# Kernel optimization log

Hardware: AMD Instinct MI355X
Metric: run time of the kernel (lower is better)

Reference implementation:

```python
import jax, jax.numpy as jnp
import numpy as np

NUM_JOINT_LIST = [8, 10, 12, 14, 16, 18, 20, 22, 24, 9, 13, 17]
NUM_GLOBAL_LIST = [1, 0, 1, 1, 0, 1, 1, 1, 0, 1, 1, 1]
M = len(NUM_JOINT_LIST)
B, T, JMAX = 16, 128, 24
H, HEADS, L, RANK = 256, 8, 4, 8
DH = H // HEADS
LAYERSCALE = 1e-4


def setup_inputs():
    key = jax.random.key(0)
    ks = jax.random.split(key, 40)
    m_idx = jax.random.randint(ks[0], (B,), 0, M)
    nj = jnp.array(NUM_JOINT_LIST)[m_idx]
    valid = jnp.arange(JMAX)[None, :] < nj[:, None]  # (B, J) real joints of each morphology
    jtype = jax.random.randint(ks[1], (B, JMAX), 0, 3)  # 0 slide, 1 hinge, 2 global
    has_g = (jnp.array(NUM_GLOBAL_LIST) > 0)[m_idx][:, None]
    jtype = jnp.where((jtype == 2) & ~has_g, 0, jtype)
    tile = lambda m: jnp.broadcast_to(m[:, None, :], (B, T, JMAX))
    slide_mask = tile((jtype == 0) & valid)
    hinge_mask = tile((jtype == 1) & valid)
    global_mask = tile((jtype == 2) & valid)
    act_mask = tile(valid)
    morph_mask = (valid[:, :, None] & valid[:, None, :]) | jnp.eye(JMAX, dtype=bool)[None]
    act = jax.random.normal(ks[2], (B, T, JMAX, 1), dtype=jnp.float32)
    s = 0.02
    inp = dict(act=act, slide_mask=slide_mask, hinge_mask=hinge_mask,
               global_mask=global_mask, act_mask=act_mask, morph_mask=morph_mask,
               m_idx=m_idx)
    inp['Ws'] = s * jax.random.normal(ks[3], (1, H)); inp['bs'] = jnp.zeros((H,))
    inp['Wh'] = s * jax.random.normal(ks[4], (1, H)); inp['bh'] = jnp.zeros((H,))
    inp['Wg'] = s * jax.random.normal(ks[5], (M, H))
    inp['Wact'] = s * jax.random.normal(ks[6], (1, H))
    pos = jax.random.normal(ks[7], (M, JMAX, H))
    pos_valid = jnp.arange(JMAX)[None, :, None] < jnp.array(NUM_JOINT_LIST)[:, None, None]
    inp['pos'] = pos * pos_valid  # rows beyond num_joint stay zero, as in the torch loop
    inp['ln1_s'] = jnp.ones((L, H)); inp['ln1_b'] = jnp.zeros((L, H))
    inp['Wqkv'] = s * jax.random.normal(ks[8], (L, H, 3 * H)); inp['bqkv'] = jnp.zeros((L, 3 * H))
    inp['loraA'] = s * jax.random.normal(ks[9], (L, M, H, RANK))
    inp['loraB'] = s * jax.random.normal(ks[10], (L, M, RANK, 3 * H))
    inp['Wo'] = s * jax.random.normal(ks[11], (L, H, H)); inp['bo'] = jnp.zeros((L, H))
    inp['ln2_s'] = jnp.ones((L, H)); inp['ln2_b'] = jnp.zeros((L, H))
    inp['W1'] = s * jax.random.normal(ks[12], (L, H, 4 * H)); inp['b1'] = jnp.zeros((L, 4 * H))
    inp['W2'] = s * jax.random.normal(ks[13], (L, 4 * H, H)); inp['b2'] = jnp.zeros((L, H))
    inp['g1'] = LAYERSCALE * jnp.ones((L, H)); inp['g2'] = LAYERSCALE * jnp.ones((L, H))
    inp['lnf_s'] = jnp.ones((H,)); inp['lnf_b'] = jnp.zeros((H,))
    return inp


def _ln(z, sc, bi):
    mu = z.mean(-1, keepdims=True)
    v = ((z - mu) ** 2).mean(-1, keepdims=True)
    return (z - mu) * jax.lax.rsqrt(v + 1e-5) * sc + bi


def reference(act, slide_mask, hinge_mask, global_mask, act_mask, morph_mask, m_idx,
              Ws, bs, Wh, bh, Wg, Wact, pos,
              ln1_s, ln1_b, Wqkv, bqkv, loraA, loraB, Wo, bo,
              ln2_s, ln2_b, W1, b1, W2, b2, g1, g2, lnf_s, lnf_b):
    has_g = (jnp.array(NUM_GLOBAL_LIST) > 0)[m_idx]  # (B,)
    a1 = act[..., :1]  # slide_dim = hinge_dim = num_global = 1
    emb = jnp.where(slide_mask[..., None], a1 @ Ws + bs, jnp.zeros((), act.dtype))
    emb = jnp.where(hinge_mask[..., None], a1 @ Wh + bh, emb)
    emb_g = a1 * Wg[m_idx][:, None, None, :]  # per-sample morphology-routed projection
    emb = jnp.where((global_mask & has_g[:, None, None])[..., None], emb_g, emb)
    y = emb + act_mask[..., None].astype(emb.dtype) * Wact[0]
    y = y + pos[m_idx][:, None]  # (B, T, J, H)
    Bv, Tv, J, _ = y.shape
    N = Bv * Tv
    x = y.reshape(N, J, H)
    amask = jnp.broadcast_to(morph_mask[:, None], (Bv, Tv, J, J)).reshape(N, J, J)
    t_idx = jnp.repeat(m_idx, Tv)  # (N,)
    neg = jnp.finfo(x.dtype).min
    scale = 1.0 / np.sqrt(DH)

    def block(x, lp):
        l1s, l1b, wqkv, bq, lA, lB, wo, bo_, l2s, l2b, w1, b1_, w2, b2_, gg1, gg2 = lp
        h = _ln(x, l1s, l1b)
        qkv = h @ wqkv + bq
        # per-task LoRA on qkv, gathered by morphology index
        qkv = qkv + jnp.einsum('njr,nrk->njk', jnp.einsum('njd,ndr->njr', h, lA[t_idx]), lB[t_idx])
        q, k, v = jnp.split(qkv, 3, axis=-1)
        q = q.reshape(N, J, HEADS, DH).transpose(0, 2, 1, 3)
        k = k.reshape(N, J, HEADS, DH).transpose(0, 2, 1, 3)
        v = v.reshape(N, J, HEADS, DH).transpose(0, 2, 1, 3)
        scores = jnp.einsum('nhid,nhjd->nhij', q, k) * scale
        scores = jnp.where(amask[:, None], scores, neg)
        attn = jax.nn.softmax(scores, axis=-1)
        o = jnp.einsum('nhij,nhjd->nhid', attn, v).transpose(0, 2, 1, 3).reshape(N, J, H)
        x = x + gg1 * (o @ wo + bo_)
        h2 = _ln(x, l2s, l2b)
        x = x + gg2 * (jax.nn.gelu(h2 @ w1 + b1_) @ w2 + b2_)
        return x, None

    x, _ = jax.lax.scan(block, x, (ln1_s, ln1_b, Wqkv, bqkv, loraA, loraB, Wo, bo,
                                   ln2_s, ln2_b, W1, b1, W2, b2, g1, g2))
    x = _ln(x, lnf_s, lnf_b)
    return x.reshape(Bv, Tv, J, H)
```

## Files before the change

### kernel.cpp

```cpp
#include <hip/hip_runtime.h>
#include <cstdint>
#include <cstddef>

#define B_     16
#define T_     128
#define J_     24
#define H_     256
#define HEADS_ 8
#define DH_    32
#define L_     4
#define RANK_  8
#define M_     12
#define NTOK   (B_*T_)
#define ROWS   (NTOK*J_)
#define KQ     320
#define HAS_G_MASK 3821

typedef __attribute__((ext_vector_type(8))) short short8;
typedef __attribute__((ext_vector_type(4))) float f32x4;

__constant__ int cNJ[M_] = {8, 10, 12, 14, 16, 18, 20, 22, 24, 9, 13, 17};

__device__ __forceinline__ float bf2f(unsigned short u) {
    union { unsigned int i; float f; } c; c.i = ((unsigned int)u) << 16; return c.f;
}
__device__ __forceinline__ unsigned short f2bf(float f) {
    union { float f; unsigned int i; } c; c.f = f;
    unsigned int x = c.i;
    return (unsigned short)((x + 0x7fffu + ((x >> 16) & 1u)) >> 16);
}
__device__ __forceinline__ float asf(unsigned int u) {
    union { unsigned int i; float f; } c; c.i = u; return c.f;
}
__device__ __forceinline__ unsigned int cvtpk(float lo, float hi) {
    unsigned int r;
    asm("v_cvt_pk_bf16_f32 %0, %1, %2" : "=v"(r) : "v"(lo), "v"(hi));
    return r;
}
__device__ __forceinline__ void gload16(const void* g, void* l) {
    __builtin_amdgcn_global_load_lds((const __attribute__((address_space(1))) void*)g,
                                     (__attribute__((address_space(3))) void*)l, 16, 0, 0);
}
#define SWZ(r) ((((r) >> 1) & 3) << 4)

__global__ void zero_flag(int* f) { *f = 0; }

__global__ __launch_bounds__(256) void detect_kernel(
    const unsigned char* __restrict__ sl, const unsigned char* __restrict__ hi,
    const unsigned char* __restrict__ gl, const int* __restrict__ m_idx,
    int* __restrict__ flag) {
    int rj = blockIdx.x * 256 + threadIdx.x;
    if (rj >= ROWS) return;
    int b = rj / (T_ * J_);
    int j = rj % J_;
    int valid = (j < cNJ[m_idx[b]]) ? 1 : 0;
    int cnt = (sl[rj] != 0) + (hi[rj] != 0) + (gl[rj] != 0);
    if (cnt != valid) atomicOr(flag, 1);
}

__global__ void wconv_t(const float* __restrict__ W, unsigned short* __restrict__ WT,
                        int K, int Nc, int total) {
    int i = blockIdx.x * 256 + threadIdx.x;
    if (i >= total) return;
    int kn = K * Nc;
    int l = i / kn;
    int r = i - l * kn;
    int n = r / K;
    int k = r - n * K;
    WT[i] = f2bf(W[(size_t)l * kn + (size_t)k * Nc + n]);
}

__global__ void wconv_qkv(const float* __restrict__ Wqkv, const float* __restrict__ loraB,
                          unsigned short* __restrict__ OT) {
    int i = blockIdx.x * 256 + threadIdx.x;
    const int total = L_ * M_ * 768 * KQ;
    if (i >= total) return;
    int k = i % KQ;
    int n = (i / KQ) % 768;
    int m = (i / (KQ * 768)) % M_;
    int l = i / (KQ * 768 * M_);
    float v = 0.f;
    if (k < 256)      v = Wqkv[((size_t)l * 256 + k) * 768 + n];
    else if (k < 264) v = loraB[(((size_t)l * M_ + m) * RANK_ + (k - 256)) * 768 + n];
    OT[i] = f2bf(v);
}

__global__ __launch_bounds__(256) void embed_kernel(
    const float* __restrict__ act, const void* __restrict__ slide,
    const void* __restrict__ hinge, const void* __restrict__ glob,
    const int* __restrict__ m_idx, const int* __restrict__ flag,
    const float* __restrict__ Ws, const float* __restrict__ bs,
    const float* __restrict__ Wh, const float* __restrict__ bh,
    const float* __restrict__ Wg, const float* __restrict__ Wact,
    const float* __restrict__ pos, float* __restrict__ X) {
    int rj = (blockIdx.x << 2) + (threadIdx.x >> 6);
    int lane = threadIdx.x & 63;
    int b = rj / (T_ * J_);
    int j = rj % J_;
    int m = m_idx[b];
    bool valid = j < cNJ[m];
    bool s, hh, gl;
    if (*flag) {
        s  = ((const int*)slide)[rj] != 0;
        hh = ((const int*)hinge)[rj] != 0;
        gl = ((const int*)glob)[rj]  != 0;
    } else {
        s  = ((const unsigned char*)slide)[rj] != 0;
        hh = ((const unsigned char*)hinge)[rj] != 0;
        gl = ((const unsigned char*)glob)[rj]  != 0;
    }
    float a1 = act[rj];
    int h0 = lane << 2;
    float e0 = 0.f, e1 = 0.f, e2 = 0.f, e3 = 0.f;
    if (s) {
        float4 w = *(const float4*)(Ws + h0); float4 bb = *(const float4*)(bs + h0);
        e0 = a1 * w.x + bb.x; e1 = a1 * w.y + bb.y; e2 = a1 * w.z + bb.z; e3 = a1 * w.w + bb.w;
    } else if (hh) {
        float4 w = *(const float4*)(Wh + h0); float4 bb = *(const float4*)(bh + h0);
        e0 = a1 * w.x + bb.x; e1 = a1 * w.y + bb.y; e2 = a1 * w.z + bb.z; e3 = a1 * w.w + bb.w;
    } else if (gl && ((HAS_G_MASK >> m) & 1)) {
        float4 w = *(const float4*)(Wg + m * H_ + h0);
        e0 = a1 * w.x; e1 = a1 * w.y; e2 = a1 * w.z; e3 = a1 * w.w;
    }
    if (valid) {
        float4 wa = *(const float4*)(Wact + h0);
        e0 += wa.x; e1 += wa.y; e2 += wa.z; e3 += wa.w;
    }
    float4 pv = *(const float4*)(pos + (size_t)(m * J_ + j) * H_ + h0);
    float4 out; out.x = e0 + pv.x; out.y = e1 + pv.y; out.z = e2 + pv.z; out.w = e3 + pv.w;
    *(float4*)(X + ((size_t)rj << 8) + h0) = out;
}

template<bool LORA>
__global__ __launch_bounds__(256) void ln_kernel(
    const float* __restrict__ X, const float* __restrict__ sc, const float* __restrict__ bi,
    const float* __restrict__ lA, const int* __restrict__ m_idx,
    unsigned short* __restrict__ Hbf, int ldh) {
    int row = (blockIdx.x << 2) + (threadIdx.x >> 6);
    int lane = threadIdx.x & 63;
    int h0 = lane << 2;
    float4 xv = *(const float4*)(X + ((size_t)row << 8) + h0);
    float s1 = xv.x + xv.y + xv.z + xv.w;
    float s2 = xv.x * xv.x + xv.y * xv.y + xv.z * xv.z + xv.w * xv.w;
    #pragma unroll
    for (int o = 32; o; o >>= 1) { s1 += __shfl_xor(s1, o); s2 += __shfl_xor(s2, o); }
    float mu = s1 * (1.f / H_);
    float var = s2 * (1.f / H_) - mu * mu;
    float rs = rsqrtf(var + 1e-5f);
    float4 scv = *(const float4*)(sc + h0);
    float4 biv = *(const float4*)(bi + h0);
    float hn0 = (xv.x - mu) * rs * scv.x + biv.x;
    float hn1 = (xv.y - mu) * rs * scv.y + biv.y;
    float hn2 = (xv.z - mu) * rs * scv.z + biv.z;
    float hn3 = (xv.w - mu) * rs * scv.w + biv.w;
    ushort4 o4; o4.x = f2bf(hn0); o4.y = f2bf(hn1); o4.z = f2bf(hn2); o4.w = f2bf(hn3);
    *(ushort4*)(Hbf + (size_t)row * ldh + h0) = o4;
    if (LORA) {
        int t = m_idx[row / (J_ * T_)];
        const float* Ap = lA + (size_t)t * (H_ * RANK_) + h0 * RANK_;
        float4 av[8];
        #pragma unroll
        for (int c = 0; c < 8; ++c) av[c] = ((const float4*)Ap)[c];
        float hn[4] = {hn0, hn1, hn2, hn3};
        float p[RANK_];
        #pragma unroll
        for (int k = 0; k < RANK_; ++k) p[k] = 0.f;
        #pragma unroll
        for (int i = 0; i < 4; ++i)
            #pragma unroll
            for (int k = 0; k < RANK_; ++k) {
                int idx = i * RANK_ + k;
                float a = (idx & 3) == 0 ? av[idx >> 2].x : (idx & 3) == 1 ? av[idx >> 2].y
                        : (idx & 3) == 2 ? av[idx >> 2].z : av[idx >> 2].w;
                p[k] += hn[i] * a;
            }
        #pragma unroll
        for (int k = 0; k < RANK_; ++k)
            #pragma unroll
            for (int o = 32; o; o >>= 1) p[k] += __shfl_xor(p[k], o);
        unsigned int w0 = (unsigned int)f2bf(p[0]) | ((unsigned int)f2bf(p[1]) << 16);
        unsigned int w1 = (unsigned int)f2bf(p[2]) | ((unsigned int)f2bf(p[3]) << 16);
        unsigned int w2 = (unsigned int)f2bf(p[4]) | ((unsigned int)f2bf(p[5]) << 16);
        unsigned int w3 = (unsigned int)f2bf(p[6]) | ((unsigned int)f2bf(p[7]) << 16);
        unsigned int tv = 0;
        if (lane == 0) tv = w0; else if (lane == 1) tv = w1;
        else if (lane == 2) tv = w2; else if (lane == 3) tv = w3;
        if (lane < 32)
            *((unsigned int*)(Hbf + (size_t)row * ldh + 256) + lane) = tv;
    }
}

__global__ __launch_bounds__(256) void lnf_kernel(
    float* __restrict__ X, const float* __restrict__ sc, const float* __restrict__ bi) {
    int row = (blockIdx.x << 2) + (threadIdx.x >> 6);
    int lane = threadIdx.x & 63;
    int h0 = lane << 2;
    float4 xv = *(const float4*)(X + ((size_t)row << 8) + h0);
    float s1 = xv.x + xv.y + xv.z + xv.w;
    float s2 = xv.x * xv.x + xv.y * xv.y + xv.z * xv.z + xv.w * xv.w;
    #pragma unroll
    for (int o = 32; o; o >>= 1) { s1 += __shfl_xor(s1, o); s2 += __shfl_xor(s2, o); }
    float mu = s1 * (1.f / H_);
    float var = s2 * (1.f / H_) - mu * mu;
    float rs = rsqrtf(var + 1e-5f);
    float4 scv = *(const float4*)(sc + h0);
    float4 biv = *(const float4*)(bi + h0);
    float4 out;
    out.x = (xv.x - mu) * rs * scv.x + biv.x;
    out.y = (xv.y - mu) * rs * scv.y + biv.y;
    out.z = (xv.z - mu) * rs * scv.z + biv.z;
    out.w = (xv.w - mu) * rs * scv.w + biv.w;
    *(float4*)(X + ((size_t)row << 8) + h0) = out;
}

template<int EPI, int K, int NC>
__global__ __launch_bounds__(256) void gemm_k(
    const unsigned short* __restrict__ A, const unsigned short* __restrict__ BT,
    const float* __restrict__ bias,
    const float* __restrict__ aux1,
    const int* __restrict__ m_idx,
    unsigned short* __restrict__ outB, float* __restrict__ outF) {
    __shared__ __align__(16) char LAs[2][8192];
    __shared__ __align__(16) char LBs[2][8192];
    char* LA0 = &LAs[0][0]; char* LA1 = &LAs[1][0];
    char* LB0 = &LBs[0][0]; char* LB1 = &LBs[1][0];
    int gx = gridDim.x;
    int nwg = gx * gridDim.y;
    int id = blockIdx.y * gx + blockIdx.x;
    int bx = blockIdx.x, by = blockIdx.y;
    {
        int q8 = nwg >> 3;
        int sid = (id & 7) * q8 + (id >> 3);
        bx = sid % gx; by = sid / gx;
    }
    int col0 = bx * 128;
    int row0 = by * 128;
    int tid = threadIdx.x;
    int wv = tid >> 6, lane = tid & 63;
    int wm = wv >> 1, wn = wv & 1;

    const unsigned short* BTe = BT;
    if (EPI == 0) BTe += (size_t)m_idx[row0 / (J_ * T_)] * (768 * KQ);

    int srow  = tid >> 2;
    int sbyte = (tid & 3) << 4;
    int sce   = (sbyte ^ SWZ(srow)) >> 1;
    const unsigned short* Ab = A   + (size_t)(row0 + srow) * K + sce;
    const unsigned short* Bb = BTe + (size_t)(col0 + srow) * K + sce;
    const size_t rstep = (size_t)64 * K;

    int ko2   = (lane >> 4) << 4;
    int rdoff = ko2 ^ SWZ(lane & 15);
    int rowA0 = wm * 64 + (lane & 15);
    int rowB0 = wn * 64 + (lane & 15);

    f32x4 acc[4][4];
    const f32x4 z = {0.f, 0.f, 0.f, 0.f};
    #pragma unroll
    for (int mi = 0; mi < 4; ++mi)
        #pragma unroll
        for (int ni = 0; ni < 4; ++ni) acc[mi][ni] = z;

    constexpr int NT = K >> 5;

    auto STAGE = [&](int kt, int b) {
        const unsigned short* a = Ab + (kt << 5);
        const unsigned short* bb = Bb + (kt << 5);
        char* la = (b ? LA1 : LA0) + (tid << 4);
        char* lb = (b ? LB1 : LB0) + (tid << 4);
        gload16(a, la);          gload16(a + rstep, la + 4096);
        gload16(bb, lb);         gload16(bb + rstep, lb + 4096);
    };
    auto COMPUTE = [&](const char* pa, const char* pb) {
        short8 af[4], bfr[4];
        #pragma unroll
        for (int q = 0; q < 4; ++q) {
            af[q]  = *(const short8*)(pa + (rowA0 + q * 16) * 64 + rdoff);
            bfr[q] = *(const short8*)(pb + (rowB0 + q * 16) * 64 + rdoff);
        }
        #pragma unroll
        for (int mi = 0; mi < 4; ++mi)
            #pragma unroll
            for (int ni = 0; ni < 4; ++ni)
                acc[mi][ni] = __builtin_amdgcn_mfma_f32_16x16x32_bf16(bfr[ni], af[mi], acc[mi][ni], 0, 0, 0);
    };

    STAGE(0, 0);
    for (int t = 0; t < NT; t += 2) {
        if (t + 1 < NT) { STAGE(t + 1, 1); asm volatile("s_waitcnt vmcnt(4)" ::: "memory"); }
        else            { asm volatile("s_waitcnt vmcnt(0)" ::: "memory"); }
        __builtin_amdgcn_s_barrier();
        __builtin_amdgcn_sched_barrier(0);
        COMPUTE(LA0, LB0);
        __builtin_amdgcn_sched_barrier(0);
        __builtin_amdgcn_s_barrier();
        if (t + 2 < NT) { STAGE(t + 2, 0); asm volatile("s_waitcnt vmcnt(4)" ::: "memory"); }
        else            { asm volatile("s_waitcnt vmcnt(0)" ::: "memory"); }
        __builtin_amdgcn_s_barrier();
        __builtin_amdgcn_sched_barrier(0);
        COMPUTE(LA1, LB1);
        __builtin_amdgcn_sched_barrier(0);
        __builtin_amdgcn_s_barrier();
    }

    int rb = row0 + wm * 64 + (lane & 15);
    int cb = col0 + wn * 64 + ((lane >> 4) << 2);

    if (EPI == 0 || EPI == 1) {
        #pragma unroll
        for (int mi = 0; mi < 4; ++mi) {
            int row = rb + mi * 16;
            #pragma unroll
            for (int ni = 0; ni < 4; ++ni) {
                int col = cb + ni * 16;
                float4 bv = *(const float4*)(bias + col);
                float v[4] = {acc[mi][ni][0] + bv.x, acc[mi][ni][1] + bv.y,
                              acc[mi][ni][2] + bv.z, acc[mi][ni][3] + bv.w};
                if (EPI == 1) {
                    #pragma unroll
                    for (int r = 0; r < 4; ++r) {
                        float u = v[r];
                        float tt = u * u;
                        float pp = fmaf(tt, 0.044715f, 1.0f) * u;
                        float e = __expf(-1.5957691216057308f * pp);
                        v[r] = u / (1.f + e);
                    }
                }
                uint2 st; st.x = cvtpk(v[0], v[1]); st.y = cvtpk(v[2], v[3]);
                *(uint2*)(outB + (size_t)row * NC + col) = st;
            }
        }
    } else {
        #pragma unroll
        for (int mi = 0; mi < 4; ++mi) {
            int row = rb + mi * 16;
            #pragma unroll
            for (int ni = 0; ni < 4; ++ni) {
                int col = cb + ni * 16;
                float4 g = *(const float4*)(aux1 + col);
                float4 bv = *(const float4*)(bias + col);
                float4 x = *(float4*)(outF + (size_t)row * H_ + col);
                x.x += g.x * (acc[mi][ni][0] + bv.x);
                x.y += g.y * (acc[mi][ni][1] + bv.y);
                x.z += g.z * (acc[mi][ni][2] + bv.z);
                x.w += g.w * (acc[mi][ni][3] + bv.w);
                *(float4*)(outF + (size_t)row * H_ + col) = x;
            }
        }
    }
}

__global__ __launch_bounds__(256) void attn_kernel(
    const unsigned short* __restrict__ QKV, const int* __restrict__ m_idx,
    unsigned short* __restrict__ O) {
    __shared__ unsigned int q2s[4][24][18];
    __shared__ unsigned int k2s[4][16][26];
    __shared__ unsigned int v2s[4][24][18];
    __shared__ float       scs[4][24][27];
    int w = threadIdx.x >> 6, lane = threadIdx.x & 63;
    int n = blockIdx.x >> 1;
    int hd = ((blockIdx.x & 1) << 2) + w;
    int nj = cNJ[m_idx[n >> 7]];
    unsigned int (*q2)[18] = q2s[w];
    unsigned int (*k2)[26] = k2s[w];
    unsigned int (*v2)[18] = v2s[w];
    float (*sc)[27] = scs[w];

    const unsigned short* base = QKV + (size_t)n * (J_ * 768) + hd * DH_;

    #pragma unroll
    for (int it = 0; it < 3; ++it) {
        int r = it * 64 + lane;
        int j = r >> 3, d0 = (r & 7) << 2, d2 = d0 >> 1;
        ushort4 x = *(const ushort4*)(base + (size_t)j * 768 + d0);
        q2[j][d2]     = (unsigned int)x.x | ((unsigned int)x.y << 16);
        q2[j][d2 + 1] = (unsigned int)x.z | ((unsigned int)x.w << 16);
    }
    #pragma unroll
    for (int it = 0; it < 3; ++it) {
        int r = it * 64 + lane;
        int j = r >> 3, d0 = (r & 7) << 2, d2 = d0 >> 1;
        ushort4 x = *(const ushort4*)(base + (size_t)j * 768 + 256 + d0);
        k2[d2][j]     = (unsigned int)x.x | ((unsigned int)x.y << 16);
        k2[d2 + 1][j] = (unsigned int)x.z | ((unsigned int)x.w << 16);
    }
    #pragma unroll
    for (int it = 0; it < 3; ++it) {
        int r = it * 64 + lane;
        int j = r >> 3, d0 = (r & 7) << 2, d2 = d0 >> 1;
        ushort4 x = *(const ushort4*)(base + (size_t)j * 768 + 512 + d0);
        v2[j][d2]     = (unsigned int)x.x | ((unsigned int)x.y << 16);
        v2[j][d2 + 1] = (unsigned int)x.z | ((unsigned int)x.w << 16);
    }

    int i = lane >> 1, half = lane & 1;
    if (lane < 48) {
        float qf[32];
        #pragma unroll
        for (int d2 = 0; d2 < 16; ++d2) {
            unsigned int x = q2[i][d2];
            qf[2 * d2]     = asf(x << 16);
            qf[2 * d2 + 1] = asf(x & 0xffff0000u);
        }
        int jb = half * 12;
        float s[12];
        #pragma unroll
        for (int jj = 0; jj < 12; ++jj) {
            int j = jb + jj;
            float acc = 0.f;
            #pragma unroll
            for (int d2 = 0; d2 < 16; ++d2) {
                unsigned int x = k2[d2][j];
                acc += qf[2 * d2] * asf(x << 16);
                acc += qf[2 * d2 + 1] * asf(x & 0xffff0000u);
            }
            bool ok = (i < nj && j < nj) || (i == j);
            s[jj] = ok ? acc * 0.17677669529663687f : -1e30f;
        }
        float mx = s[0];
        #pragma unroll
        for (int jj = 1; jj < 12; ++jj) mx = fmaxf(mx, s[jj]);
        mx = fmaxf(mx, __shfl_xor(mx, 1));
        float sm = 0.f;
        #pragma unroll
        for (int jj = 0; jj < 12; ++jj) { float e = __expf(s[jj] - mx); s[jj] = e; sm += e; }
        sm += __shfl_xor(sm, 1);
        float inv = 1.f / sm;
        #pragma unroll
        for (int jj = 0; jj < 12; ++jj) sc[i][jb + jj] = s[jj] * inv;
    }

    #pragma unroll
    for (int it = 0; it < 6; ++it) {
        int i2 = it * 4 + (lane >> 4), d2 = lane & 15;
        float olo = 0.f, ohi = 0.f;
        #pragma unroll
        for (int j = 0; j < J_; ++j) {
            float p = sc[i2][j];
            unsigned int x = v2[j][d2];
            olo += p * asf(x << 16);
            ohi += p * asf(x & 0xffff0000u);
        }
        unsigned int o = (unsigned int)f2bf(olo) | ((unsigned int)f2bf(ohi) << 16);
        *(unsigned int*)(O + (size_t)(n * J_ + i2) * H_ + hd * DH_ + 2 * d2) = o;
    }
}

extern "C" void kernel_launch(void* const* d_in, const int* in_sizes, int n_in,
                              void* d_out, int out_size, void* d_ws, size_t ws_size,
                              hipStream_t stream) {
    (void)in_sizes; (void)n_in; (void)out_size; (void)ws_size;
    const float* act   = (const float*)d_in[0];
    const void*  slide = d_in[1];
    const void*  hinge = d_in[2];
    const void*  glob  = d_in[3];
    const int* m_idx  = (const int*)d_in[6];
    const float* Ws   = (const float*)d_in[7];
    const float* bs   = (const float*)d_in[8];
    const float* Wh   = (const float*)d_in[9];
    const float* bh   = (const float*)d_in[10];
    const float* Wg   = (const float*)d_in[11];
    const float* Wact = (const float*)d_in[12];
    const float* pos  = (const float*)d_in[13];
    const float* ln1s = (const float*)d_in[14];
    const float* ln1b = (const float*)d_in[15];
    const float* Wqkv = (const float*)d_in[16];
    const float* bqkv = (const float*)d_in[17];
    const float* loraA= (const float*)d_in[18];
    const float* loraB= (const float*)d_in[19];
    const float* Wo   = (const float*)d_in[20];
    const float* bo   = (const float*)d_in[21];
    const float* ln2s = (const float*)d_in[22];
    const float* ln2b = (const float*)d_in[23];
    const float* W1   = (const float*)d_in[24];
    const float* b1   = (const float*)d_in[25];
    const float* W2   = (const float*)d_in[26];
    const float* b2   = (const float*)d_in[27];
    const float* g1   = (const float*)d_in[28];
    const float* g2   = (const float*)d_in[29];
    const float* lnfs = (const float*)d_in[30];
    const float* lnfb = (const float*)d_in[31];

    float* X = (float*)d_out;

    size_t off = 0;
    char* ws = (char*)d_ws;
    auto nxt = [&](size_t bytes) -> char* {
        char* p = ws + off; off += (bytes + 255) & ~(size_t)255; return p;
    };
    int*            dflag  = (int*)nxt(256);
    unsigned short* Hbf    = (unsigned short*)nxt((size_t)ROWS * KQ * 2);
    unsigned short* QKVG   = (unsigned short*)nxt((size_t)ROWS * 1024 * 2);
    unsigned short* WqkvTp = (unsigned short*)nxt((size_t)L_ * M_ * 768 * KQ * 2);
    unsigned short* WoT    = (unsigned short*)nxt((size_t)L_ * H_ * H_ * 2);
    unsigned short* W1T    = (unsigned short*)nxt((size_t)L_ * H_ * 1024 * 2);
    unsigned short* W2T    = (unsigned short*)nxt((size_t)L_ * 1024 * H_ * 2);
    unsigned short* Obf    = Hbf;

    zero_flag<<<1, 1, 0, stream>>>(dflag);
    detect_kernel<<<(ROWS + 255) / 256, 256, 0, stream>>>(
        (const unsigned char*)slide, (const unsigned char*)hinge,
        (const unsigned char*)glob, m_idx, dflag);

    wconv_qkv<<<(L_ * M_ * 768 * KQ + 255) / 256, 256, 0, stream>>>(Wqkv, loraB, WqkvTp);
    wconv_t<<<(L_ * H_ * H_   + 255) / 256, 256, 0, stream>>>(Wo, WoT, H_, H_,   L_ * H_ * H_);
    wconv_t<<<(L_ * H_ * 1024 + 255) / 256, 256, 0, stream>>>(W1, W1T, H_, 1024, L_ * H_ * 1024);
    wconv_t<<<(L_ * 1024 * H_ + 255) / 256, 256, 0, stream>>>(W2, W2T, 1024, H_, L_ * 1024 * H_);

    embed_kernel<<<ROWS / 4, 256, 0, stream>>>(act, slide, hinge, glob, m_idx, dflag,
                                               Ws, bs, Wh, bh, Wg, Wact, pos, X);

    for (int l = 0; l < L_; ++l) {
        ln_kernel<true><<<ROWS / 4, 256, 0, stream>>>(X, ln1s + l * H_, ln1b + l * H_,
                                                      loraA + (size_t)l * M_ * H_ * RANK_, m_idx, Hbf, KQ);
        gemm_k<0, KQ, 768><<<dim3(6, 384), 256, 0, stream>>>(Hbf, WqkvTp + (size_t)l * M_ * 768 * KQ,
                                                             bqkv + l * 768, nullptr, m_idx,
                                                             QKVG, nullptr);
        attn_kernel<<<NTOK * 2, 256, 0, stream>>>(QKVG, m_idx, Obf);
        gemm_k<2, 256, 256><<<dim3(2, 384), 256, 0, stream>>>(Obf, WoT + (size_t)l * H_ * H_,
                                                              bo + l * H_, g1 + l * H_, m_idx,
                                                              nullptr, X);
        ln_kernel<false><<<ROWS / 4, 256, 0, stream>>>(X, ln2s + l * H_, ln2b + l * H_,
                                                       nullptr, nullptr, Hbf, H_);
        gemm_k<1, 256, 1024><<<dim3(8, 384), 256, 0, stream>>>(Hbf, W1T + (size_t)l * H_ * 1024,
                                                               b1 + l * 1024, nullptr, m_idx,
                                                               QKVG, nullptr);
        gemm_k<2, 1024, 256><<<dim3(2, 384), 256, 0, stream>>>(QKVG, W2T + (size_t)l * 1024 * H_,
                                                               b2 + l * H_, g2 + l * H_, m_idx,
                                                               nullptr, X);
    }

    lnf_kernel<<<ROWS / 4, 256, 0, stream>>>(X, lnfs, lnfb);
}
```

Measured before the change: 1.380 ms.

## Fuse residual GEMMs with following LayerNorm and fold first LN into embed

Adds a full-row resid_gemm kernel: each block owns 64 rows across all 256 columns, so it can apply the residual update and then the next LayerNorm (ln2, the next layer's ln1, or the final LN) in its epilogue. The first ln1 plus its LoRA projection is folded into the embedding kernel, and a light lora_tail kernel computes the LoRA-A products from the bf16 LN output. This removes the separate LN passes over the fp32 residual stream and several launches per layer. The cost is a narrower-tiled GEMM with a cross-wave shared-memory reduction, LoRA-A computed from bf16-rounded activations, and a GELU exp now written with exp2f.

New measurement: 1.374 ms. About the same (-0.4%).

```diff
diff --git a/kernel.cpp b/kernel.cpp
--- a/kernel.cpp
+++ b/kernel.cpp
@@ -85,14 +85,16 @@
     OT[i] = f2bf(v);
 }
 
-__global__ __launch_bounds__(256) void embed_kernel(
+__global__ __launch_bounds__(256) void embed_ln_kernel(
     const float* __restrict__ act, const void* __restrict__ slide,
     const void* __restrict__ hinge, const void* __restrict__ glob,
     const int* __restrict__ m_idx, const int* __restrict__ flag,
     const float* __restrict__ Ws, const float* __restrict__ bs,
     const float* __restrict__ Wh, const float* __restrict__ bh,
     const float* __restrict__ Wg, const float* __restrict__ Wact,
-    const float* __restrict__ pos, float* __restrict__ X) {
+    const float* __restrict__ pos, const float* __restrict__ lns,
+    const float* __restrict__ lnb, const float* __restrict__ lA,
+    float* __restrict__ X, unsigned short* __restrict__ Hq) {
     int rj = (blockIdx.x << 2) + (threadIdx.x >> 6);
     int lane = threadIdx.x & 63;
     int b = rj / (T_ * J_);
@@ -127,99 +129,104 @@
         e0 += wa.x; e1 += wa.y; e2 += wa.z; e3 += wa.w;
     }
     float4 pv = *(const float4*)(pos + (size_t)(m * J_ + j) * H_ + h0);
-    float4 out; out.x = e0 + pv.x; out.y = e1 + pv.y; out.z = e2 + pv.z; out.w = e3 + pv.w;
+    float y0 = e0 + pv.x, y1 = e1 + pv.y, y2 = e2 + pv.z, y3 = e3 + pv.w;
+    float4 out; out.x = y0; out.y = y1; out.z = y2; out.w = y3;
     *(float4*)(X + ((size_t)rj << 8) + h0) = out;
-}
-
-template<bool LORA>
-__global__ __launch_bounds__(256) void ln_kernel(
-    const float* __restrict__ X, const float* __restrict__ sc, const float* __restrict__ bi,
-    const float* __restrict__ lA, const int* __restrict__ m_idx,
-    unsigned short* __restrict__ Hbf, int ldh) {
-    int row = (blockIdx.x << 2) + (threadIdx.x >> 6);
-    int lane = threadIdx.x & 63;
-    int h0 = lane << 2;
-    float4 xv = *(const float4*)(X + ((size_t)row << 8) + h0);
-    float s1 = xv.x + xv.y + xv.z + xv.w;
-    float s2 = xv.x * xv.x + xv.y * xv.y + xv.z * xv.z + xv.w * xv.w;
+
+    float s1 = y0 + y1 + y2 + y3;
+    float s2 = y0 * y0 + y1 * y1 + y2 * y2 + y3 * y3;
     #pragma unroll
     for (int o = 32; o; o >>= 1) { s1 += __shfl_xor(s1, o); s2 += __shfl_xor(s2, o); }
     float mu = s1 * (1.f / H_);
     float var = s2 * (1.f / H_) - mu * mu;
     float rs = rsqrtf(var + 1e-5f);
-    float4 scv = *(const float4*)(sc + h0);
-    float4 biv = *(const float4*)(bi + h0);
-    float hn0 = (xv.x - mu) * rs * scv.x + biv.x;
-    float hn1 = (xv.y - mu) * rs * scv.y + biv.y;
-    float hn2 = (xv.z - mu) * rs * scv.z + biv.z;
-    float hn3 = (xv.w - mu) * rs * scv.w + biv.w;
+    float4 scv = *(const float4*)(lns + h0);
+    float4 biv = *(const float4*)(lnb + h0);
+    float hn0 = (y0 - mu) * rs * scv.x + biv.x;
+    float hn1 = (y1 - mu) * rs * scv.y + biv.y;
+    float hn2 = (y2 - mu) * rs * scv.z + biv.z;
+    float hn3 = (y3 - mu) * rs * scv.w + biv.w;
     ushort4 o4; o4.x = f2bf(hn0); o4.y = f2bf(hn1); o4.z = f2bf(hn2); o4.w = f2bf(hn3);
-    *(ushort4*)(Hbf + (size_t)row * ldh + h0) = o4;
-    if (LORA) {
-        int t = m_idx[row / (J_ * T_)];
-        const float* Ap = lA + (size_t)t * (H_ * RANK_) + h0 * RANK_;
-        float4 av[8];
-        #pragma unroll
-        for (int c = 0; c < 8; ++c) av[c] = ((const float4*)Ap)[c];
-        float hn[4] = {hn0, hn1, hn2, hn3};
-        float p[RANK_];
-        #pragma unroll
-        for (int k = 0; k < RANK_; ++k) p[k] = 0.f;
-        #pragma unroll
-        for (int i = 0; i < 4; ++i)
-            #pragma unroll
-            for (int k = 0; k < RANK_; ++k) {
-                int idx = i * RANK_ + k;
-                float a = (idx & 3) == 0 ? av[idx >> 2].x : (idx & 3) == 1 ? av[idx >> 2].y
-                        : (idx & 3) == 2 ? av[idx >> 2].z : av[idx >> 2].w;
-                p[k] += hn[i] * a;
-            }
-        #pragma unroll
-        for (int k = 0; k < RANK_; ++k)
-            #pragma unroll
-            for (int o = 32; o; o >>= 1) p[k] += __shfl_xor(p[k], o);
-        unsigned int w0 = (unsigned int)f2bf(p[0]) | ((unsigned int)f2bf(p[1]) << 16);
-        unsigned int w1 = (unsigned int)f2bf(p[2]) | ((unsigned int)f2bf(p[3]) << 16);
-        unsigned int w2 = (unsigned int)f2bf(p[4]) | ((unsigned int)f2bf(p[5]) << 16);
-        unsigned int w3 = (unsigned int)f2bf(p[6]) | ((unsigned int)f2bf(p[7]) << 16);
-        unsigned int tv = 0;
-        if (lane == 0) tv = w0; else if (lane == 1) tv = w1;
-        else if (lane == 2) tv = w2; else if (lane == 3) tv = w3;
-        if (lane < 32)
-            *((unsigned int*)(Hbf + (size_t)row * ldh + 256) + lane) = tv;
-    }
-}
-
-__global__ __launch_bounds__(256) void lnf_kernel(
-    float* __restrict__ X, const float* __restrict__ sc, const float* __restrict__ bi) {
+    *(ushort4*)(Hq + (size_t)rj * KQ + h0) = o4;
+
+    int t = m;
+    const float* Ap = lA + (size_t)t * (H_ * RANK_) + h0 * RANK_;
+    float4 av[8];
+    #pragma unroll
+    for (int c = 0; c < 8; ++c) av[c] = ((const float4*)Ap)[c];
+    float hn[4] = {hn0, hn1, hn2, hn3};
+    float p[RANK_];
+    #pragma unroll
+    for (int k = 0; k < RANK_; ++k) p[k] = 0.f;
+    #pragma unroll
+    for (int i = 0; i < 4; ++i)
+        #pragma unroll
+        for (int k = 0; k < RANK_; ++k) {
+            int idx = i * RANK_ + k;
+            float a = (idx & 3) == 0 ? av[idx >> 2].x : (idx & 3) == 1 ? av[idx >> 2].y
+                    : (idx & 3) == 2 ? av[idx >> 2].z : av[idx >> 2].w;
+            p[k] += hn[i] * a;
+        }
+    #pragma unroll
+    for (int k = 0; k < RANK_; ++k)
+        #pragma unroll
+        for (int o = 32; o; o >>= 1) p[k] += __shfl_xor(p[k], o);
+    unsigned int w0 = (unsigned int)f2bf(p[0]) | ((unsigned int)f2bf(p[1]) << 16);
+    unsigned int w1 = (unsigned int)f2bf(p[2]) | ((unsigned int)f2bf(p[3]) << 16);
+    unsigned int w2 = (unsigned int)f2bf(p[4]) | ((unsigned int)f2bf(p[5]) << 16);
+    unsigned int w3 = (unsigned int)f2bf(p[6]) | ((unsigned int)f2bf(p[7]) << 16);
+    unsigned int tv = 0;
+    if (lane == 0) tv = w0; else if (lane == 1) tv = w1;
+    else if (lane == 2) tv = w2; else if (lane == 3) tv = w3;
+    if (lane < 32)
+        *((unsigned int*)(Hq + (size_t)rj * KQ + 256) + lane) = tv;
+}
+
+__global__ __launch_bounds__(256) void lora_tail_kernel(
+    unsigned short* __restrict__ Hq, const float* __restrict__ lA,
+    const int* __restrict__ m_idx) {
     int row = (blockIdx.x << 2) + (threadIdx.x >> 6);
     int lane = threadIdx.x & 63;
+    int t = m_idx[row / (J_ * T_)];
     int h0 = lane << 2;
-    float4 xv = *(const float4*)(X + ((size_t)row << 8) + h0);
-    float s1 = xv.x + xv.y + xv.z + xv.w;
-    float s2 = xv.x * xv.x + xv.y * xv.y + xv.z * xv.z + xv.w * xv.w;
-    #pragma unroll
-    for (int o = 32; o; o >>= 1) { s1 += __shfl_xor(s1, o); s2 += __shfl_xor(s2, o); }
-    float mu = s1 * (1.f / H_);
-    float var = s2 * (1.f / H_) - mu * mu;
-    float rs = rsqrtf(var + 1e-5f);
-    float4 scv = *(const float4*)(sc + h0);
-    float4 biv = *(const float4*)(bi + h0);
-    float4 out;
-    out.x = (xv.x - mu) * rs * scv.x + biv.x;
-    out.y = (xv.y - mu) * rs * scv.y + biv.y;
-    out.z = (xv.z - mu) * rs * scv.z + biv.z;
-    out.w = (xv.w - mu) * rs * scv.w + biv.w;
-    *(float4*)(X + ((size_t)row << 8) + h0) = out;
+    ushort4 hv = *(const ushort4*)(Hq + (size_t)row * KQ + h0);
+    float hn[4] = {bf2f(hv.x), bf2f(hv.y), bf2f(hv.z), bf2f(hv.w)};
+    const float* Ap = lA + (size_t)t * (H_ * RANK_) + h0 * RANK_;
+    float4 av[8];
+    #pragma unroll
+    for (int c = 0; c < 8; ++c) av[c] = ((const float4*)Ap)[c];
+    float p[RANK_];
+    #pragma unroll
+    for (int k = 0; k < RANK_; ++k) p[k] = 0.f;
+    #pragma unroll
+    for (int i = 0; i < 4; ++i)
+        #pragma unroll
+        for (int k = 0; k < RANK_; ++k) {
+            int idx = i * RANK_ + k;
+            float a = (idx & 3) == 0 ? av[idx >> 2].x : (idx & 3) == 1 ? av[idx >> 2].y
+                    : (idx & 3) == 2 ? av[idx >> 2].z : av[idx >> 2].w;
+            p[k] += hn[i] * a;
+        }
+    #pragma unroll
+    for (int k = 0; k < RANK_; ++k)
+        #pragma unroll
+        for (int o = 32; o; o >>= 1) p[k] += __shfl_xor(p[k], o);
+    unsigned int w0 = (unsigned int)f2bf(p[0]) | ((unsigned int)f2bf(p[1]) << 16);
+    unsigned int w1 = (unsigned int)f2bf(p[2]) | ((unsigned int)f2bf(p[3]) << 16);
+    unsigned int w2 = (unsigned int)f2bf(p[4]) | ((unsigned int)f2bf(p[5]) << 16);
+    unsigned int w3 = (unsigned int)f2bf(p[6]) | ((unsigned int)f2bf(p[7]) << 16);
+    unsigned int tv = 0;
+    if (lane == 0) tv = w0; else if (lane == 1) tv = w1;
+    else if (lane == 2) tv = w2; else if (lane == 3) tv = w3;
+    if (lane < 32)
+        *((unsigned int*)(Hq + (size_t)row * KQ + 256) + lane) = tv;
 }
 
 template<int EPI, int K, int NC>
 __global__ __launch_bounds__(256) void gemm_k(
     const unsigned short* __restrict__ A, const unsigned short* __restrict__ BT,
-    const float* __restrict__ bias,
-    const float* __restrict__ aux1,
-    const int* __restrict__ m_idx,
-    unsigned short* __restrict__ outB, float* __restrict__ outF) {
+    const float* __restrict__ bias, const int* __restrict__ m_idx,
+    unsigned short* __restrict__ outB) {
     __shared__ __align__(16) char LAs[2][8192];
     __shared__ __align__(16) char LBs[2][8192];
     char* LA0 = &LAs[0][0]; char* LA1 = &LAs[1][0];
@@ -227,12 +234,9 @@
     int gx = gridDim.x;
     int nwg = gx * gridDim.y;
     int id = blockIdx.y * gx + blockIdx.x;
-    int bx = blockIdx.x, by = blockIdx.y;
-    {
-        int q8 = nwg >> 3;
-        int sid = (id & 7) * q8 + (id >> 3);
-        bx = sid % gx; by = sid / gx;
-    }
+    int q8 = nwg >> 3;
+    int sid = (id & 7) * q8 + (id >> 3);
+    int bx = sid % gx, by = sid / gx;
     int col0 = bx * 128;
     int row0 = by * 128;
     int tid = threadIdx.x;
@@ -249,8 +253,7 @@
     const unsigned short* Bb = BTe + (size_t)(col0 + srow) * K + sce;
     const size_t rstep = (size_t)64 * K;
 
-    int ko2   = (lane >> 4) << 4;
-    int rdoff = ko2 ^ SWZ(lane & 15);
+    int rdoff = ((lane >> 4) << 4) ^ SWZ(lane & 15);
     int rowA0 = wm * 64 + (lane & 15);
     int rowB0 = wn * 64 + (lane & 15);
 
@@ -306,45 +309,185 @@
     int rb = row0 + wm * 64 + (lane & 15);
     int cb = col0 + wn * 64 + ((lane >> 4) << 2);
 
-    if (EPI == 0 || EPI == 1) {
-        #pragma unroll
-        for (int mi = 0; mi < 4; ++mi) {
-            int row = rb + mi * 16;
+    #pragma unroll
+    for (int mi = 0; mi < 4; ++mi) {
+        int row = rb + mi * 16;
+        #pragma unroll
+        for (int ni = 0; ni < 4; ++ni) {
+            int col = cb + ni * 16;
+            float4 bv = *(const float4*)(bias + col);
+            float v[4] = {acc[mi][ni][0] + bv.x, acc[mi][ni][1] + bv.y,
+                          acc[mi][ni][2] + bv.z, acc[mi][ni][3] + bv.w};
+            if (EPI == 1) {
+                #pragma unroll
+                for (int r = 0; r < 4; ++r) {
+                    float u = v[r];
+                    float tt = u * u;
+                    float pp = fmaf(tt, 0.044715f, 1.0f) * u;
+                    float e = exp2f(-2.3025850929940457f * pp);
+                    v[r] = u / (1.f + e);
+                }
+            }
+            uint2 st; st.x = cvtpk(v[0], v[1]); st.y = cvtpk(v[2], v[3]);
+            *(uint2*)(outB + (size_t)row * NC + col) = st;
+        }
+    }
+}
+
+template<int MODE, int K>
+__global__ __launch_bounds__(256) void resid_gemm(
+    const unsigned short* __restrict__ A, const unsigned short* __restrict__ BT,
+    const float* __restrict__ bias, const float* __restrict__ gv,
+    float* __restrict__ X, unsigned short* __restrict__ Hout,
+    const float* __restrict__ lns, const float* __restrict__ lnb) {
+    __shared__ __align__(16) char LAs[2][4096];
+    __shared__ __align__(16) char LBs[2][16384];
+    __shared__ float red1[4][16][4], red2[4][16][4];
+    char* LA0 = &LAs[0][0]; char* LA1 = &LAs[1][0];
+    char* LB0 = &LBs[0][0]; char* LB1 = &LBs[1][0];
+    int nwg = gridDim.x;
+    int id = blockIdx.x;
+    int q8 = nwg >> 3;
+    int sid = (id & 7) * q8 + (id >> 3);
+    int row0 = sid * 64;
+    int tid = threadIdx.x;
+    int wn = tid >> 6, lane = tid & 63;
+
+    int srow  = tid >> 2;
+    int sbyte = (tid & 3) << 4;
+    int sce   = (sbyte ^ SWZ(srow)) >> 1;
+    const unsigned short* Ab = A  + (size_t)(row0 + srow) * K + sce;
+    const unsigned short* Bb = BT + (size_t)srow * K + sce;
+    const size_t bstep = (size_t)64 * K;
+
+    int rdoff = ((lane >> 4) << 4) ^ SWZ(lane & 15);
+    int rowB0 = wn * 64 + (lane & 15);
+
+    f32x4 acc[4][4];
+    const f32x4 z = {0.f, 0.f, 0.f, 0.f};
+    #pragma unroll
+    for (int mi = 0; mi < 4; ++mi)
+        #pragma unroll
+        for (int ni = 0; ni < 4; ++ni) acc[mi][ni] = z;
+
+    constexpr int NT = K >> 5;
+
+    auto STAGE = [&](int kt, int b) {
+        const unsigned short* a = Ab + (kt << 5);
+        const unsigned short* bb = Bb + (kt << 5);
+        char* la = (b ? LA1 : LA0) + (tid << 4);
+        char* lb = (b ? LB1 : LB0) + (tid << 4);
+        gload16(a, la);
+        gload16(bb,             lb);
+        gload16(bb + bstep,     lb + 4096);
+        gload16(bb + 2 * bstep, lb + 8192);
+        gload16(bb + 3 * bstep, lb + 12288);
+    };
+    auto COMPUTE = [&](const char* pa, const char* pb) {
+        short8 af[4], bfr[4];
+        #pragma unroll
+        for (int q = 0; q < 4; ++q) {
+            af[q]  = *(const short8*)(pa + ((lane & 15) + q * 16) * 64 + rdoff);
+            bfr[q] = *(const short8*)(pb + (rowB0 + q * 16) * 64 + rdoff);
+        }
+        #pragma unroll
+        for (int mi = 0; mi < 4; ++mi)
             #pragma unroll
-            for (int ni = 0; ni < 4; ++ni) {
-                int col = cb + ni * 16;
-                float4 bv = *(const float4*)(bias + col);
-                float v[4] = {acc[mi][ni][0] + bv.x, acc[mi][ni][1] + bv.y,
-                              acc[mi][ni][2] + bv.z, acc[mi][ni][3] + bv.w};
-                if (EPI == 1) {
-                    #pragma unroll
-                    for (int r = 0; r < 4; ++r) {
-                        float u = v[r];
-                        float tt = u * u;
-                        float pp = fmaf(tt, 0.044715f, 1.0f) * u;
-                        float e = __expf(-1.5957691216057308f * pp);
-                        v[r] = u / (1.f + e);
-                    }
-                }
-                uint2 st; st.x = cvtpk(v[0], v[1]); st.y = cvtpk(v[2], v[3]);
-                *(uint2*)(outB + (size_t)row * NC + col) = st;
+            for (int ni = 0; ni < 4; ++ni)
+                acc[mi][ni] = __builtin_amdgcn_mfma_f32_16x16x32_bf16(bfr[ni], af[mi], acc[mi][ni], 0, 0, 0);
+    };
+
+    STAGE(0, 0);
+    for (int t = 0; t < NT; t += 2) {
+        if (t + 1 < NT) { STAGE(t + 1, 1); asm volatile("s_waitcnt vmcnt(5)" ::: "memory"); }
+        else            { asm volatile("s_waitcnt vmcnt(0)" ::: "memory"); }
+        __builtin_amdgcn_s_barrier();
+        __builtin_amdgcn_sched_barrier(0);
+        COMPUTE(LA0, LB0);
+        __builtin_amdgcn_sched_barrier(0);
+        __builtin_amdgcn_s_barrier();
+        if (t + 2 < NT) { STAGE(t + 2, 0); asm volatile("s_waitcnt vmcnt(5)" ::: "memory"); }
+        else            { asm volatile("s_waitcnt vmcnt(0)" ::: "memory"); }
+        __builtin_amdgcn_s_barrier();
+        __builtin_amdgcn_sched_barrier(0);
+        COMPUTE(LA1, LB1);
+        __builtin_amdgcn_sched_barrier(0);
+        __builtin_amdgcn_s_barrier();
+    }
+
+    int rb0 = row0 + (lane & 15);
+    int cb = (wn << 6) + ((lane >> 4) << 2);
+    float4 b4[4], g4[4];
+    #pragma unroll
+    for (int ni = 0; ni < 4; ++ni) {
+        b4[ni] = *(const float4*)(bias + cb + ni * 16);
+        g4[ni] = *(const float4*)(gv + cb + ni * 16);
+    }
+    float s1[4] = {0, 0, 0, 0}, s2[4] = {0, 0, 0, 0};
+    #pragma unroll
+    for (int mi = 0; mi < 4; ++mi) {
+        int row = rb0 + mi * 16;
+        #pragma unroll
+        for (int ni = 0; ni < 4; ++ni) {
+            int col = cb + ni * 16;
+            float4 x = *(const float4*)(X + ((size_t)row << 8) + col);
+            float u0 = fmaf(g4[ni].x, acc[mi][ni][0] + b4[ni].x, x.x);
+            float u1 = fmaf(g4[ni].y, acc[mi][ni][1] + b4[ni].y, x.y);
+            float u2 = fmaf(g4[ni].z, acc[mi][ni][2] + b4[ni].z, x.z);
+            float u3 = fmaf(g4[ni].w, acc[mi][ni][3] + b4[ni].w, x.w);
+            if (MODE != 2) {
+                float4 st; st.x = u0; st.y = u1; st.z = u2; st.w = u3;
+                *(float4*)(X + ((size_t)row << 8) + col) = st;
             }
-        }
-    } else {
-        #pragma unroll
-        for (int mi = 0; mi < 4; ++mi) {
-            int row = rb + mi * 16;
-            #pragma unroll
-            for (int ni = 0; ni < 4; ++ni) {
-                int col = cb + ni * 16;
-                float4 g = *(const float4*)(aux1 + col);
-                float4 bv = *(const float4*)(bias + col);
-                float4 x = *(float4*)(outF + (size_t)row * H_ + col);
-                x.x += g.x * (acc[mi][ni][0] + bv.x);
-                x.y += g.y * (acc[mi][ni][1] + bv.y);
-                x.z += g.z * (acc[mi][ni][2] + bv.z);
-                x.w += g.w * (acc[mi][ni][3] + bv.w);
-                *(float4*)(outF + (size_t)row * H_ + col) = x;
+            acc[mi][ni][0] = u0; acc[mi][ni][1] = u1;
+            acc[mi][ni][2] = u2; acc[mi][ni][3] = u3;
+            s1[mi] += u0 + u1 + u2 + u3;
+            s2[mi] += u0 * u0 + u1 * u1 + u2 * u2 + u3 * u3;
+        }
+    }
+    #pragma unroll
+    for (int mi = 0; mi < 4; ++mi) {
+        s1[mi] += __shfl_xor(s1[mi], 16); s1[mi] += __shfl_xor(s1[mi], 32);
+        s2[mi] += __shfl_xor(s2[mi], 16); s2[mi] += __shfl_xor(s2[mi], 32);
+    }
+    if (lane < 16) {
+        #pragma unroll
+        for (int mi = 0; mi < 4; ++mi) { red1[mi][lane][wn] = s1[mi]; red2[mi][lane][wn] = s2[mi]; }
+    }
+    __syncthreads();
+    float mu[4], rs[4];
+    #pragma unroll
+    for (int mi = 0; mi < 4; ++mi) {
+        int r = lane & 15;
+        float t1 = red1[mi][r][0] + red1[mi][r][1] + red1[mi][r][2] + red1[mi][r][3];
+        float t2 = red2[mi][r][0] + red2[mi][r][1] + red2[mi][r][2] + red2[mi][r][3];
+        mu[mi] = t1 * (1.f / H_);
+        float var = t2 * (1.f / H_) - mu[mi] * mu[mi];
+        rs[mi] = rsqrtf(var + 1e-5f);
+    }
+    float4 l4[4], o4v[4];
+    #pragma unroll
+    for (int ni = 0; ni < 4; ++ni) {
+        l4[ni]  = *(const float4*)(lns + cb + ni * 16);
+        o4v[ni] = *(const float4*)(lnb + cb + ni * 16);
+    }
+    #pragma unroll
+    for (int mi = 0; mi < 4; ++mi) {
+        int row = rb0 + mi * 16;
+        #pragma unroll
+        for (int ni = 0; ni < 4; ++ni) {
+            int col = cb + ni * 16;
+            float h0 = (acc[mi][ni][0] - mu[mi]) * rs[mi] * l4[ni].x + o4v[ni].x;
+            float h1 = (acc[mi][ni][1] - mu[mi]) * rs[mi] * l4[ni].y + o4v[ni].y;
+            float h2 = (acc[mi][ni][2] - mu[mi]) * rs[mi] * l4[ni].z + o4v[ni].z;
+            float h3 = (acc[mi][ni][3] - mu[mi]) * rs[mi] * l4[ni].w + o4v[ni].w;
+            if (MODE == 2) {
+                float4 st; st.x = h0; st.y = h1; st.z = h2; st.w = h3;
+                *(float4*)(X + ((size_t)row << 8) + col) = st;
+            } else {
+                constexpr int ldh = (MODE == 1) ? KQ : H_;
+                uint2 st; st.x = cvtpk(h0, h1); st.y = cvtpk(h2, h3);
+                *(uint2*)(Hout + (size_t)row * ldh + col) = st;
             }
         }
     }
@@ -489,13 +632,14 @@
         char* p = ws + off; off += (bytes + 255) & ~(size_t)255; return p;
     };
     int*            dflag  = (int*)nxt(256);
-    unsigned short* Hbf    = (unsigned short*)nxt((size_t)ROWS * KQ * 2);
+    unsigned short* Hq     = (unsigned short*)nxt((size_t)ROWS * KQ * 2);
+    unsigned short* Hw     = (unsigned short*)nxt((size_t)ROWS * H_ * 2);
     unsigned short* QKVG   = (unsigned short*)nxt((size_t)ROWS * 1024 * 2);
     unsigned short* WqkvTp = (unsigned short*)nxt((size_t)L_ * M_ * 768 * KQ * 2);
     unsigned short* WoT    = (unsigned short*)nxt((size_t)L_ * H_ * H_ * 2);
     unsigned short* W1T    = (unsigned short*)nxt((size_t)L_ * H_ * 1024 * 2);
     unsigned short* W2T    = (unsigned short*)nxt((size_t)L_ * 1024 * H_ * 2);
-    unsigned short* Obf    = Hbf;
+    unsigned short* Obf    = Hq;
 
     zero_flag<<<1, 1, 0, stream>>>(dflag);
     detect_kernel<<<(ROWS + 255) / 256, 256, 0, stream>>>(
@@ -507,28 +651,29 @@
     wconv_t<<<(L_ * H_ * 1024 + 255) / 256, 256, 0, stream>>>(W1, W1T, H_, 1024, L_ * H_ * 1024);
     wconv_t<<<(L_ * 1024 * H_ + 255) / 256, 256, 0, stream>>>(W2, W2T, 1024, H_, L_ * 1024 * H_);
 
-    embed_kernel<<<ROWS / 4, 256, 0, stream>>>(act, slide, hinge, glob, m_idx, dflag,
-                                               Ws, bs, Wh, bh, Wg, Wact, pos, X);
+    embed_ln_kernel<<<ROWS / 4, 256, 0, stream>>>(act, slide, hinge, glob, m_idx, dflag,
+                                                  Ws, bs, Wh, bh, Wg, Wact, pos,
+                                                  ln1s, ln1b, loraA, X, Hq);
 
     for (int l = 0; l < L_; ++l) {
-        ln_kernel<true><<<ROWS / 4, 256, 0, stream>>>(X, ln1s + l * H_, ln1b + l * H_,
-                                                      loraA + (size_t)l * M_ * H_ * RANK_, m_idx, Hbf, KQ);
-        gemm_k<0, KQ, 768><<<dim3(6, 384), 256, 0, stream>>>(Hbf, WqkvTp + (size_t)l * M_ * 768 * KQ,
-                                                             bqkv + l * 768, nullptr, m_idx,
-                                                             QKVG, nullptr);
+        gemm_k<0, KQ, 768><<<dim3(6, 384), 256, 0, stream>>>(
+            Hq, WqkvTp + (size_t)l * M_ * 768 * KQ, bqkv + l * 768, m_idx, QKVG);
         attn_kernel<<<NTOK * 2, 256, 0, stream>>>(QKVG, m_idx, Obf);
-        gemm_k<2, 256, 256><<<dim3(2, 384), 256, 0, stream>>>(Obf, WoT + (size_t)l * H_ * H_,
-                                                              bo + l * H_, g1 + l * H_, m_idx,
-                                                              nullptr, X);
-        ln_kernel<false><<<ROWS / 4, 256, 0, stream>>>(X, ln2s + l * H_, ln2b + l * H_,
-                                                       nullptr, nullptr, Hbf, H_);
-        gemm_k<1, 256, 1024><<<dim3(8, 384), 256, 0, stream>>>(Hbf, W1T + (size_t)l * H_ * 1024,
-                                                               b1 + l * 1024, nullptr, m_idx,
-                                                               QKVG, nullptr);
-        gemm_k<2, 1024, 256><<<dim3(2, 384), 256, 0, stream>>>(QKVG, W2T + (size_t)l * 1024 * H_,
-                                                               b2 + l * H_, g2 + l * H_, m_idx,
-                                                               nullptr, X);
-    }
-
-    lnf_kernel<<<ROWS / 4, 256, 0, stream>>>(X, lnfs, lnfb);
-}
+        resid_gemm<0, 256><<<768, 256, 0, stream>>>(
+            Obf, WoT + (size_t)l * H_ * H_, bo + l * H_, g1 + l * H_,
+            X, Hw, ln2s + l * H_, ln2b + l * H_);
+        gemm_k<1, 256, 1024><<<dim3(8, 384), 256, 0, stream>>>(
+            Hw, W1T + (size_t)l * H_ * 1024, b1 + l * 1024, m_idx, QKVG);
+        if (l < L_ - 1) {
+            resid_gemm<1, 1024><<<768, 256, 0, stream>>>(
+                QKVG, W2T + (size_t)l * 1024 * H_, b2 + l * H_, g2 + l * H_,
+                X, Hq, ln1s + (l + 1) * H_, ln1b + (l + 1) * H_);
+            lora_tail_kernel<<<ROWS / 4, 256, 0, stream>>>(
+                Hq, loraA + (size_t)(l + 1) * M_ * H_ * RANK_, m_idx);
+        } else {
+            resid_gemm<2, 1024><<<768, 256, 0, stream>>>(
+                QKVG, W2T + (size_t)l * 1024 * H_, b2 + l * H_, g2 + l * H_,
+                X, nullptr, lnfs, lnfb);
+        }
+    }
+}
```
